# Kernel tuning notes

Measured on AMD Instinct MI355X. Metric: run time of the kernel, lower is better.

The kernel has to match this reference:

```python
import jax, jax.numpy as jnp
import numpy as np

B, S, D = 2, 2048, 1024
H = 16
HD = D // H  # head_dim = 64


def setup_inputs() -> dict:
    key = jax.random.key(0)
    ks = jax.random.split(key, 9)
    std = 1.0 / np.sqrt(HD)
    inp = {
        "X": jax.random.normal(ks[0], (B, S, D), dtype=jnp.float32),
        # per-head Q/K/V Linear weights stacked: [H, head_dim, head_dim], biases [H, head_dim]
        "Wq": jax.random.uniform(ks[1], (H, HD, HD), jnp.float32, -std, std),
        "bq": jax.random.uniform(ks[2], (H, HD), jnp.float32, -std, std),
        "Wk": jax.random.uniform(ks[3], (H, HD, HD), jnp.float32, -std, std),
        "bk": jax.random.uniform(ks[4], (H, HD), jnp.float32, -std, std),
        "Wv": jax.random.uniform(ks[5], (H, HD, HD), jnp.float32, -std, std),
        "bv": jax.random.uniform(ks[6], (H, HD), jnp.float32, -std, std),
        # output projection: [D, D] (in, out layout), bias [D]
        "Wo": jax.random.uniform(ks[7], (D, D), jnp.float32, -1.0 / np.sqrt(D), 1.0 / np.sqrt(D)),
        "bo": jax.random.uniform(ks[8], (D,), jnp.float32, -1.0 / np.sqrt(D), 1.0 / np.sqrt(D)),
    }
    return inp


def reference(X, Wq, bq, Wk, bk, Wv, bv, Wo, bo):
    # Split hidden dim into heads: [B, S, H, HD]
    x = X.reshape(B, S, H, HD)
    scale = jnp.sqrt(jnp.asarray(HD, dtype=X.dtype))
    # Per-head linear projections (batched over heads)
    Q = jnp.einsum("bshd,hde->bshe", x, Wq) + bq
    K = jnp.einsum("bshd,hde->bshe", x, Wk) + bk
    V = jnp.einsum("bshd,hde->bshe", x, Wv) + bv
    # Attention scores [B, H, S, S]
    scores = jnp.einsum("bshd,bthd->bhst", Q, K) / scale
    attn = jax.nn.softmax(scores, axis=-1)
    # Weighted values -> [B, S, H, HD] -> concat -> [B, S, D]
    out = jnp.einsum("bhst,bthd->bshd", attn, V).reshape(B, S, D)
    return out @ Wo + bo
```

## Files before the change

### kernel.cpp

```cpp
#include <hip/hip_runtime.h>
#include <stdint.h>

#define B_  2
#define S_  2048
#define D_  1024
#define H_  16
#define HD_ 64
#define TOK (B_*S_)

typedef __bf16 bf16x8 __attribute__((ext_vector_type(8)));
typedef __bf16 bf16x4 __attribute__((ext_vector_type(4)));
typedef float  f32x4  __attribute__((ext_vector_type(4)));

static_assert(sizeof(bf16x8) == 16, "bf16x8 must be 16B");
static_assert(sizeof(bf16x4) == 8,  "bf16x4 must be 8B");

__device__ __forceinline__ float fexp2(float x) { return __builtin_amdgcn_exp2f(x); }

__device__ __forceinline__ f32x4 mfma16(bf16x8 a, bf16x8 b, f32x4 c) {
    return __builtin_amdgcn_mfma_f32_16x16x32_bf16(a, b, c, 0, 0, 0);
}

__global__ __launch_bounds__(256) void k_transpose_wo(
    const float* __restrict__ Wo, unsigned short* __restrict__ WoT)
{
    __shared__ float t[64][65];
    const int i0 = blockIdx.x * 64;
    const int o0 = blockIdx.y * 64;
    const int tid = threadIdx.x;
    #pragma unroll
    for (int p = 0; p < 16; ++p) {
        int idx = tid + p * 256;
        int r = idx >> 6, c = idx & 63;
        t[r][c] = Wo[(size_t)(i0 + r) * D_ + o0 + c];
    }
    __syncthreads();
    #pragma unroll
    for (int p = 0; p < 16; ++p) {
        int idx = tid + p * 256;
        int r = idx >> 6, c = idx & 63;
        reinterpret_cast<__bf16*>(WoT)[(size_t)(o0 + r) * D_ + i0 + c] = (__bf16)t[c][r];
    }
}

__global__ __launch_bounds__(256) void k_qkv(
    const float* __restrict__ X,
    const float* __restrict__ Wq, const float* __restrict__ bq,
    const float* __restrict__ Wk, const float* __restrict__ bk,
    const float* __restrict__ Wv, const float* __restrict__ bv,
    unsigned short* __restrict__ Qo, unsigned short* __restrict__ Ko,
    unsigned short* __restrict__ Vt)
{
    __shared__ float          Wf[64][65];
    __shared__ unsigned short Xl[128 * 64];
    __shared__ unsigned short Wl[64 * 64];

    const int tid  = threadIdx.x;
    const int lane = tid & 63, w = tid >> 6;
    const int g = lane >> 4, q = lane & 15;
    const int tok0 = blockIdx.x * 128;
    const int h    = blockIdx.y;
    const int z    = blockIdx.z;
    const float* W  = (z == 0) ? Wq : (z == 1) ? Wk : Wv;
    const float* bb = (z == 0) ? bq : (z == 1) ? bk : bv;

    #pragma unroll
    for (int i = 0; i < 4; ++i) {
        int c = tid + 256 * i;
        int r = c >> 4, c4 = (c & 15) * 4;
        *reinterpret_cast<float4*>(&Wf[r][c4]) =
            *reinterpret_cast<const float4*>(&W[h * 4096 + r * 64 + c4]);
    }
    #pragma unroll
    for (int i = 0; i < 4; ++i) {
        int c = tid + 256 * i;
        int row = c >> 3, slot = c & 7;
        const float* src = &X[(size_t)(tok0 + row) * D_ + h * HD_ + slot * 8];
        float4 x0 = *reinterpret_cast<const float4*>(src);
        float4 x1 = *reinterpret_cast<const float4*>(src + 4);
        bf16x8 v = { (__bf16)x0.x, (__bf16)x0.y, (__bf16)x0.z, (__bf16)x0.w,
                     (__bf16)x1.x, (__bf16)x1.y, (__bf16)x1.z, (__bf16)x1.w };
        *reinterpret_cast<bf16x8*>(
            reinterpret_cast<char*>(Xl) + row * 128 + ((slot ^ (row & 7)) * 16)) = v;
    }
    __syncthreads();

    #pragma unroll
    for (int i = 0; i < 2; ++i) {
        int c = tid + 256 * i;
        int e = c >> 3, slot = c & 7;
        bf16x8 v;
        #pragma unroll
        for (int j = 0; j < 8; ++j) v[j] = (__bf16)Wf[slot * 8 + j][e];
        *reinterpret_cast<bf16x8*>(
            reinterpret_cast<char*>(Wl) + e * 128 + ((slot ^ (e & 7)) * 16)) = v;
    }
    __syncthreads();

    f32x4 acc[2][4] = {};
    #pragma unroll
    for (int s = 0; s < 2; ++s) {
        bf16x8 af[2], bfr[4];
        #pragma unroll
        for (int am = 0; am < 2; ++am) {
            int row  = w * 32 + am * 16 + q;
            int slot = (s * 4 + g) ^ (row & 7);
            af[am] = *reinterpret_cast<const bf16x8*>(
                reinterpret_cast<const char*>(Xl) + row * 128 + slot * 16);
        }
        #pragma unroll
        for (int bn = 0; bn < 4; ++bn) {
            int row  = bn * 16 + q;
            int slot = (s * 4 + g) ^ (row & 7);
            bfr[bn] = *reinterpret_cast<const bf16x8*>(
                reinterpret_cast<const char*>(Wl) + row * 128 + slot * 16);
        }
        #pragma unroll
        for (int am = 0; am < 2; ++am)
            #pragma unroll
            for (int bn = 0; bn < 4; ++bn)
                acc[am][bn] = mfma16(af[am], bfr[bn], acc[am][bn]);
    }

    const float scq = 0.18033688011112042f;
    const int b  = tok0 >> 11;
    const int sb = (tok0 & (S_ - 1)) + w * 32;
    #pragma unroll
    for (int bn = 0; bn < 4; ++bn) {
        int e = bn * 16 + q;
        float bia = bb[h * HD_ + e];
        #pragma unroll
        for (int am = 0; am < 2; ++am) {
            int s4 = sb + am * 16 + 4 * g;
            if (z == 2) {
                bf16x4 ov = { (__bf16)(acc[am][bn][0] + bia), (__bf16)(acc[am][bn][1] + bia),
                              (__bf16)(acc[am][bn][2] + bia), (__bf16)(acc[am][bn][3] + bia) };
                *reinterpret_cast<bf16x4*>(
                    &Vt[((size_t)(b * H_ + h) * HD_ + e) * S_ + s4]) = ov;
            } else {
                float sc = (z == 0) ? scq : 1.0f;
                unsigned short* dst = (z == 0) ? Qo : Ko;
                __bf16* d16 = reinterpret_cast<__bf16*>(dst);
                #pragma unroll
                for (int j = 0; j < 4; ++j)
                    d16[((size_t)(b * H_ + h) * S_ + s4 + j) * HD_ + e] =
                        (__bf16)((acc[am][bn][j] + bia) * sc);
            }
        }
    }
}

__global__ __launch_bounds__(256) void k_attn(
    const unsigned short* __restrict__ Q,
    const unsigned short* __restrict__ K,
    const unsigned short* __restrict__ V,
    unsigned short* __restrict__ O)
{
    __shared__ unsigned short K_lds[2][32 * 72];
    __shared__ unsigned short V_lds[2][64 * 40];
    __shared__ unsigned short P_lds[4][16 * 40];

    const int bh = blockIdx.y;
    const unsigned short* Qp = Q + (size_t)bh * S_ * HD_;
    const unsigned short* Kp = K + (size_t)bh * S_ * HD_;
    const unsigned short* Vp = V + (size_t)bh * HD_ * S_;

    const int tid  = threadIdx.x;
    const int lane = tid & 63, w = tid >> 6;
    const int g = lane >> 4, q = lane & 15;
    const int q0 = blockIdx.x * 64 + w * 16;

    bf16x8 qf0 = *reinterpret_cast<const bf16x8*>(&Qp[(size_t)(q0 + q) * HD_ + 8 * g]);
    bf16x8 qf1 = *reinterpret_cast<const bf16x8*>(&Qp[(size_t)(q0 + q) * HD_ + 32 + 8 * g]);

    f32x4 acc0 = {0.f, 0.f, 0.f, 0.f}, acc1 = acc0, acc2 = acc0, acc3 = acc0;
    float m = -3.0e38f, lp = 0.0f;

    const int kr = tid >> 3, ks = (tid & 7) * 8;
    const int vr = tid >> 2, vs = (tid & 3) * 8;
    unsigned short* Pw = P_lds[w];

    const unsigned short* kSrc = Kp + (size_t)kr * HD_ + ks;
    const unsigned short* vSrc = Vp + (size_t)vr * S_  + vs;

    {
        uint4 k0 = *reinterpret_cast<const uint4*>(kSrc);
        uint4 v0 = *reinterpret_cast<const uint4*>(vSrc);
        *reinterpret_cast<uint4*>(&K_lds[0][kr * 72 + ks]) = k0;
        *reinterpret_cast<uint4*>(&V_lds[0][vr * 40 + vs]) = v0;
    }
    __syncthreads();

    const int NT = S_ / 32;
    for (int t = 0; t < NT; ++t) {
        const int cur = t & 1, nxt = cur ^ 1;

        uint4 kn, vn;
        const bool more = (t + 1 < NT);
        if (more) {
            kn = *reinterpret_cast<const uint4*>(kSrc + (size_t)(t + 1) * 32 * HD_);
            vn = *reinterpret_cast<const uint4*>(vSrc + (size_t)(t + 1) * 32);
        }

        const unsigned short* Kb = K_lds[cur];
        const unsigned short* Vb = V_lds[cur];
        bf16x8 k00 = *reinterpret_cast<const bf16x8*>(&Kb[q * 72 + 8 * g]);
        bf16x8 k01 = *reinterpret_cast<const bf16x8*>(&Kb[q * 72 + 32 + 8 * g]);
        bf16x8 k10 = *reinterpret_cast<const bf16x8*>(&Kb[(16 + q) * 72 + 8 * g]);
        bf16x8 k11 = *reinterpret_cast<const bf16x8*>(&Kb[(16 + q) * 72 + 32 + 8 * g]);
        bf16x8 vf0 = *reinterpret_cast<const bf16x8*>(&Vb[(0 * 16 + q) * 40 + 8 * g]);
        bf16x8 vf1 = *reinterpret_cast<const bf16x8*>(&Vb[(1 * 16 + q) * 40 + 8 * g]);
        bf16x8 vf2 = *reinterpret_cast<const bf16x8*>(&Vb[(2 * 16 + q) * 40 + 8 * g]);
        bf16x8 vf3 = *reinterpret_cast<const bf16x8*>(&Vb[(3 * 16 + q) * 40 + 8 * g]);

        f32x4 z4 = {0.f, 0.f, 0.f, 0.f};
        f32x4 s0 = mfma16(k00, qf0, z4); s0 = mfma16(k01, qf1, s0);
        f32x4 s1 = mfma16(k10, qf0, z4); s1 = mfma16(k11, qf1, s1);

        float pmax = fmaxf(fmaxf(fmaxf(s0[0], s0[1]), fmaxf(s0[2], s0[3])),
                           fmaxf(fmaxf(s1[0], s1[1]), fmaxf(s1[2], s1[3])));
        if (!__all(pmax - m <= 8.0f)) {
            float pm = pmax;
            pm = fmaxf(pm, __shfl_xor(pm, 16));
            pm = fmaxf(pm, __shfl_xor(pm, 32));
            float mn  = fmaxf(m, pm);
            float scl = fexp2(m - mn);
            m = mn;
            lp *= scl;
            acc0 *= scl; acc1 *= scl; acc2 *= scl; acc3 *= scl;
        }
        float p0 = fexp2(s0[0] - m), p1 = fexp2(s0[1] - m);
        float p2 = fexp2(s0[2] - m), p3 = fexp2(s0[3] - m);
        float p4 = fexp2(s1[0] - m), p5 = fexp2(s1[1] - m);
        float p6 = fexp2(s1[2] - m), p7 = fexp2(s1[3] - m);
        lp += ((p0 + p1) + (p2 + p3)) + ((p4 + p5) + (p6 + p7));

        bf16x4 pa = { (__bf16)p0, (__bf16)p1, (__bf16)p2, (__bf16)p3 };
        bf16x4 pb = { (__bf16)p4, (__bf16)p5, (__bf16)p6, (__bf16)p7 };
        *reinterpret_cast<bf16x4*>(&Pw[q * 40 + 4 * g])      = pa;
        *reinterpret_cast<bf16x4*>(&Pw[q * 40 + 16 + 4 * g]) = pb;

        bf16x8 pf = *reinterpret_cast<const bf16x8*>(&Pw[q * 40 + 8 * g]);
        acc0 = mfma16(vf0, pf, acc0);
        acc1 = mfma16(vf1, pf, acc1);
        acc2 = mfma16(vf2, pf, acc2);
        acc3 = mfma16(vf3, pf, acc3);

        if (more) {
            *reinterpret_cast<uint4*>(&K_lds[nxt][kr * 72 + ks]) = kn;
            *reinterpret_cast<uint4*>(&V_lds[nxt][vr * 40 + vs]) = vn;
        }
        __syncthreads();
    }

    lp += __shfl_xor(lp, 16);
    lp += __shfl_xor(lp, 32);
    const float inv = 1.0f / lp;
    const int b = bh >> 4, h = bh & 15;
    size_t row = (size_t)(b * S_ + q0 + q) * D_ + h * HD_ + 4 * g;
    __bf16* Ob = reinterpret_cast<__bf16*>(O);
    bf16x4 o0 = { (__bf16)(acc0[0]*inv), (__bf16)(acc0[1]*inv),
                  (__bf16)(acc0[2]*inv), (__bf16)(acc0[3]*inv) };
    bf16x4 o1 = { (__bf16)(acc1[0]*inv), (__bf16)(acc1[1]*inv),
                  (__bf16)(acc1[2]*inv), (__bf16)(acc1[3]*inv) };
    bf16x4 o2 = { (__bf16)(acc2[0]*inv), (__bf16)(acc2[1]*inv),
                  (__bf16)(acc2[2]*inv), (__bf16)(acc2[3]*inv) };
    bf16x4 o3 = { (__bf16)(acc3[0]*inv), (__bf16)(acc3[1]*inv),
                  (__bf16)(acc3[2]*inv), (__bf16)(acc3[3]*inv) };
    *reinterpret_cast<bf16x4*>(&Ob[row + 0])  = o0;
    *reinterpret_cast<bf16x4*>(&Ob[row + 16]) = o1;
    *reinterpret_cast<bf16x4*>(&Ob[row + 32]) = o2;
    *reinterpret_cast<bf16x4*>(&Ob[row + 48]) = o3;
}

__global__ __launch_bounds__(256) void k_out(
    const unsigned short* __restrict__ A,
    const unsigned short* __restrict__ Wt,
    const float* __restrict__ bo,
    float* __restrict__ C)
{
    __shared__ unsigned short Al[2][128 * 64];
    __shared__ unsigned short Bl[2][128 * 64];

    const int tid  = threadIdx.x;
    const int lane = tid & 63, w = tid >> 6;
    const int g = lane >> 4, q = lane & 15;
    const int wr = w & 1, wc = w >> 1;
    const int m0 = blockIdx.x * 128;
    const int n0 = blockIdx.y * 128;

    int    sbyte[4];
    size_t sgA[4], sgB[4];
    #pragma unroll
    for (int i = 0; i < 4; ++i) {
        int c = tid + 256 * i;
        int row = c >> 3, slot = c & 7;
        sbyte[i] = row * 128 + ((slot ^ (row & 7)) * 16);
        sgA[i] = (size_t)(m0 + row) * D_ + slot * 8;
        sgB[i] = (size_t)(n0 + row) * D_ + slot * 8;
    }

    uint4 ra[4], rb[4];
    #pragma unroll
    for (int i = 0; i < 4; ++i) {
        ra[i] = *reinterpret_cast<const uint4*>(A  + sgA[i]);
        rb[i] = *reinterpret_cast<const uint4*>(Wt + sgB[i]);
    }
    #pragma unroll
    for (int i = 0; i < 4; ++i) {
        *reinterpret_cast<uint4*>(reinterpret_cast<char*>(Al[0]) + sbyte[i]) = ra[i];
        *reinterpret_cast<uint4*>(reinterpret_cast<char*>(Bl[0]) + sbyte[i]) = rb[i];
    }
    __syncthreads();

    f32x4 acc[4][4] = {};
    const int NKT = D_ / 64;
    for (int kt = 0; kt < NKT; ++kt) {
        const int cur = kt & 1, nxt = cur ^ 1;
        const bool more = (kt + 1 < NKT);
        if (more) {
            #pragma unroll
            for (int i = 0; i < 4; ++i) {
                ra[i] = *reinterpret_cast<const uint4*>(A  + sgA[i] + (kt + 1) * 64);
                rb[i] = *reinterpret_cast<const uint4*>(Wt + sgB[i] + (kt + 1) * 64);
            }
        }
        const char* Ab = reinterpret_cast<const char*>(Al[cur]);
        const char* Bb = reinterpret_cast<const char*>(Bl[cur]);
        #pragma unroll
        for (int s = 0; s < 2; ++s) {
            bf16x8 af[4], bfr[4];
            #pragma unroll
            for (int am = 0; am < 4; ++am) {
                int row  = wr * 64 + am * 16 + q;
                int slot = (s * 4 + g) ^ (row & 7);
                af[am] = *reinterpret_cast<const bf16x8*>(Ab + row * 128 + slot * 16);
            }
            #pragma unroll
            for (int bn = 0; bn < 4; ++bn) {
                int row  = wc * 64 + bn * 16 + q;
                int slot = (s * 4 + g) ^ (row & 7);
                bfr[bn] = *reinterpret_cast<const bf16x8*>(Bb + row * 128 + slot * 16);
            }
            #pragma unroll
            for (int am = 0; am < 4; ++am)
                #pragma unroll
                for (int bn = 0; bn < 4; ++bn)
                    acc[am][bn] = mfma16(af[am], bfr[bn], acc[am][bn]);
        }
        if (more) {
            #pragma unroll
            for (int i = 0; i < 4; ++i) {
                *reinterpret_cast<uint4*>(reinterpret_cast<char*>(Al[nxt]) + sbyte[i]) = ra[i];
                *reinterpret_cast<uint4*>(reinterpret_cast<char*>(Bl[nxt]) + sbyte[i]) = rb[i];
            }
        }
        __syncthreads();
    }

    #pragma unroll
    for (int bn = 0; bn < 4; ++bn) {
        int n = n0 + wc * 64 + bn * 16 + q;
        float bia = bo[n];
        #pragma unroll
        for (int am = 0; am < 4; ++am) {
            int mbase = m0 + wr * 64 + am * 16 + 4 * g;
            #pragma unroll
            for (int j = 0; j < 4; ++j)
                C[(size_t)(mbase + j) * D_ + n] = acc[am][bn][j] + bia;
        }
    }
}

extern "C" void kernel_launch(void* const* d_in, const int* in_sizes, int n_in,
                              void* d_out, int out_size, void* d_ws, size_t ws_size,
                              hipStream_t stream)
{
    const float* X  = (const float*)d_in[0];
    const float* Wq = (const float*)d_in[1];
    const float* bq = (const float*)d_in[2];
    const float* Wk = (const float*)d_in[3];
    const float* bk = (const float*)d_in[4];
    const float* Wv = (const float*)d_in[5];
    const float* bv = (const float*)d_in[6];
    const float* Wo = (const float*)d_in[7];
    const float* bo = (const float*)d_in[8];
    float* out = (float*)d_out;

    unsigned short* ws = (unsigned short*)d_ws;
    const size_t QN = (size_t)B_ * H_ * S_ * HD_;
    unsigned short* Qb  = ws;
    unsigned short* Kb  = ws + QN;
    unsigned short* Vtb = ws + 2 * QN;
    unsigned short* Ob  = ws + 3 * QN;
    unsigned short* WoT = ws + 4 * QN;

    k_transpose_wo<<<dim3(16, 16), 256, 0, stream>>>(Wo, WoT);
    k_qkv<<<dim3(TOK / 128, H_, 3), 256, 0, stream>>>(X, Wq, bq, Wk, bk, Wv, bv, Qb, Kb, Vtb);
    k_attn<<<dim3(S_ / 64, B_ * H_), 256, 0, stream>>>(Qb, Kb, Vtb, Ob);
    k_out<<<dim3(TOK / 128, D_ / 128), 256, 0, stream>>>(Ob, WoT, bo, out);
}
```

Measured before the change: 180.9 us.

## Fuse Q/K/V projections per block and process two query tiles per attention wave

The QKV projection now loads and converts each X tile once and computes Q, K and V in one block, using weights pre-transposed to bf16 by a new small kernel. This removes the repeated X reads and the per-block weight transpose. Q/K stores are vectorized by swapping MFMA operand order. The attention kernel gives each wave 32 query rows instead of 16, reusing each K/V LDS fragment across two query tiles. That halves the grid and raises register and LDS pressure per block.

Result: slower. 186.7 us (+3.2%).

```diff
diff --git a/kernel.cpp b/kernel.cpp
--- a/kernel.cpp
+++ b/kernel.cpp
@@ -43,34 +43,49 @@
     }
 }
 
+__global__ __launch_bounds__(256) void k_transpose_w(
+    const float* __restrict__ Wq, const float* __restrict__ Wk,
+    const float* __restrict__ Wv, unsigned short* __restrict__ WT)
+{
+    __shared__ float t[64][65];
+    const int h = blockIdx.x, z = blockIdx.y;
+    const float* W = (z == 0) ? Wq : (z == 1) ? Wk : Wv;
+    const int tid = threadIdx.x;
+    #pragma unroll
+    for (int p = 0; p < 4; ++p) {
+        int idx = tid + p * 256;
+        int r = idx >> 4, c4 = (idx & 15) * 4;
+        *reinterpret_cast<float4*>(&t[r][c4]) =
+            *reinterpret_cast<const float4*>(&W[h * 4096 + r * 64 + c4]);
+    }
+    __syncthreads();
+    const int e = tid >> 2, db = (tid & 3) * 16;
+    __bf16* out = reinterpret_cast<__bf16*>(WT) + ((size_t)(z * H_ + h) * 64 + e) * 64 + db;
+    #pragma unroll
+    for (int jj = 0; jj < 2; ++jj) {
+        bf16x8 v;
+        #pragma unroll
+        for (int j = 0; j < 8; ++j) v[j] = (__bf16)t[db + jj * 8 + j][e];
+        *reinterpret_cast<bf16x8*>(out + jj * 8) = v;
+    }
+}
+
 __global__ __launch_bounds__(256) void k_qkv(
-    const float* __restrict__ X,
-    const float* __restrict__ Wq, const float* __restrict__ bq,
-    const float* __restrict__ Wk, const float* __restrict__ bk,
-    const float* __restrict__ Wv, const float* __restrict__ bv,
+    const float* __restrict__ X, const unsigned short* __restrict__ WT,
+    const float* __restrict__ bq, const float* __restrict__ bk,
+    const float* __restrict__ bv,
     unsigned short* __restrict__ Qo, unsigned short* __restrict__ Ko,
     unsigned short* __restrict__ Vt)
 {
-    __shared__ float          Wf[64][65];
     __shared__ unsigned short Xl[128 * 64];
-    __shared__ unsigned short Wl[64 * 64];
+    __shared__ unsigned short Wl[3][64 * 64];
 
     const int tid  = threadIdx.x;
     const int lane = tid & 63, w = tid >> 6;
     const int g = lane >> 4, q = lane & 15;
     const int tok0 = blockIdx.x * 128;
     const int h    = blockIdx.y;
-    const int z    = blockIdx.z;
-    const float* W  = (z == 0) ? Wq : (z == 1) ? Wk : Wv;
-    const float* bb = (z == 0) ? bq : (z == 1) ? bk : bv;
-
-    #pragma unroll
-    for (int i = 0; i < 4; ++i) {
-        int c = tid + 256 * i;
-        int r = c >> 4, c4 = (c & 15) * 4;
-        *reinterpret_cast<float4*>(&Wf[r][c4]) =
-            *reinterpret_cast<const float4*>(&W[h * 4096 + r * 64 + c4]);
-    }
+
     #pragma unroll
     for (int i = 0; i < 4; ++i) {
         int c = tid + 256 * i;
@@ -83,68 +98,89 @@
         *reinterpret_cast<bf16x8*>(
             reinterpret_cast<char*>(Xl) + row * 128 + ((slot ^ (row & 7)) * 16)) = v;
     }
+    #pragma unroll
+    for (int zz = 0; zz < 3; ++zz) {
+        #pragma unroll
+        for (int i = 0; i < 2; ++i) {
+            int c = tid + 256 * i;
+            int e = c >> 3, slot = c & 7;
+            bf16x8 v = *reinterpret_cast<const bf16x8*>(
+                &WT[((size_t)(zz * H_ + h) * 64 + e) * 64 + slot * 8]);
+            *reinterpret_cast<bf16x8*>(
+                reinterpret_cast<char*>(Wl[zz]) + e * 128 + ((slot ^ (e & 7)) * 16)) = v;
+        }
+    }
     __syncthreads();
-
-    #pragma unroll
-    for (int i = 0; i < 2; ++i) {
-        int c = tid + 256 * i;
-        int e = c >> 3, slot = c & 7;
-        bf16x8 v;
-        #pragma unroll
-        for (int j = 0; j < 8; ++j) v[j] = (__bf16)Wf[slot * 8 + j][e];
-        *reinterpret_cast<bf16x8*>(
-            reinterpret_cast<char*>(Wl) + e * 128 + ((slot ^ (e & 7)) * 16)) = v;
-    }
-    __syncthreads();
-
-    f32x4 acc[2][4] = {};
-    #pragma unroll
-    for (int s = 0; s < 2; ++s) {
-        bf16x8 af[2], bfr[4];
-        #pragma unroll
-        for (int am = 0; am < 2; ++am) {
-            int row  = w * 32 + am * 16 + q;
-            int slot = (s * 4 + g) ^ (row & 7);
-            af[am] = *reinterpret_cast<const bf16x8*>(
-                reinterpret_cast<const char*>(Xl) + row * 128 + slot * 16);
-        }
-        #pragma unroll
-        for (int bn = 0; bn < 4; ++bn) {
-            int row  = bn * 16 + q;
-            int slot = (s * 4 + g) ^ (row & 7);
-            bfr[bn] = *reinterpret_cast<const bf16x8*>(
-                reinterpret_cast<const char*>(Wl) + row * 128 + slot * 16);
-        }
-        #pragma unroll
-        for (int am = 0; am < 2; ++am)
-            #pragma unroll
-            for (int bn = 0; bn < 4; ++bn)
-                acc[am][bn] = mfma16(af[am], bfr[bn], acc[am][bn]);
-    }
 
     const float scq = 0.18033688011112042f;
     const int b  = tok0 >> 11;
     const int sb = (tok0 & (S_ - 1)) + w * 32;
-    #pragma unroll
-    for (int bn = 0; bn < 4; ++bn) {
-        int e = bn * 16 + q;
-        float bia = bb[h * HD_ + e];
+
+    #pragma unroll
+    for (int z = 0; z < 3; ++z) {
+        const float* bb = (z == 0) ? bq : (z == 1) ? bk : bv;
+        f32x4 acc[2][4] = {};
         #pragma unroll
-        for (int am = 0; am < 2; ++am) {
-            int s4 = sb + am * 16 + 4 * g;
+        for (int s = 0; s < 2; ++s) {
+            bf16x8 af[2], bfr[4];
+            #pragma unroll
+            for (int am = 0; am < 2; ++am) {
+                int row  = w * 32 + am * 16 + q;
+                int slot = (s * 4 + g) ^ (row & 7);
+                af[am] = *reinterpret_cast<const bf16x8*>(
+                    reinterpret_cast<const char*>(Xl) + row * 128 + slot * 16);
+            }
+            #pragma unroll
+            for (int bn = 0; bn < 4; ++bn) {
+                int row  = bn * 16 + q;
+                int slot = (s * 4 + g) ^ (row & 7);
+                bfr[bn] = *reinterpret_cast<const bf16x8*>(
+                    reinterpret_cast<const char*>(Wl[z]) + row * 128 + slot * 16);
+            }
             if (z == 2) {
-                bf16x4 ov = { (__bf16)(acc[am][bn][0] + bia), (__bf16)(acc[am][bn][1] + bia),
-                              (__bf16)(acc[am][bn][2] + bia), (__bf16)(acc[am][bn][3] + bia) };
-                *reinterpret_cast<bf16x4*>(
-                    &Vt[((size_t)(b * H_ + h) * HD_ + e) * S_ + s4]) = ov;
+                #pragma unroll
+                for (int am = 0; am < 2; ++am)
+                    #pragma unroll
+                    for (int bn = 0; bn < 4; ++bn)
+                        acc[am][bn] = mfma16(af[am], bfr[bn], acc[am][bn]);
             } else {
-                float sc = (z == 0) ? scq : 1.0f;
-                unsigned short* dst = (z == 0) ? Qo : Ko;
-                __bf16* d16 = reinterpret_cast<__bf16*>(dst);
                 #pragma unroll
-                for (int j = 0; j < 4; ++j)
-                    d16[((size_t)(b * H_ + h) * S_ + s4 + j) * HD_ + e] =
-                        (__bf16)((acc[am][bn][j] + bia) * sc);
+                for (int am = 0; am < 2; ++am)
+                    #pragma unroll
+                    for (int bn = 0; bn < 4; ++bn)
+                        acc[am][bn] = mfma16(bfr[bn], af[am], acc[am][bn]);
+            }
+        }
+        if (z == 2) {
+            #pragma unroll
+            for (int bn = 0; bn < 4; ++bn) {
+                int e = bn * 16 + q;
+                float bia = bb[h * HD_ + e];
+                #pragma unroll
+                for (int am = 0; am < 2; ++am) {
+                    int s4 = sb + am * 16 + 4 * g;
+                    bf16x4 ov = { (__bf16)(acc[am][bn][0] + bia), (__bf16)(acc[am][bn][1] + bia),
+                                  (__bf16)(acc[am][bn][2] + bia), (__bf16)(acc[am][bn][3] + bia) };
+                    *reinterpret_cast<bf16x4*>(
+                        &Vt[((size_t)(b * H_ + h) * HD_ + e) * S_ + s4]) = ov;
+                }
+            }
+        } else {
+            const float sc = (z == 0) ? scq : 1.0f;
+            unsigned short* dst = (z == 0) ? Qo : Ko;
+            #pragma unroll
+            for (int bn = 0; bn < 4; ++bn) {
+                float4 bia4 = *reinterpret_cast<const float4*>(&bb[h * HD_ + bn * 16 + 4 * g]);
+                #pragma unroll
+                for (int am = 0; am < 2; ++am) {
+                    int tok = sb + am * 16 + q;
+                    bf16x4 ov = { (__bf16)((acc[am][bn][0] + bia4.x) * sc),
+                                  (__bf16)((acc[am][bn][1] + bia4.y) * sc),
+                                  (__bf16)((acc[am][bn][2] + bia4.z) * sc),
+                                  (__bf16)((acc[am][bn][3] + bia4.w) * sc) };
+                    *reinterpret_cast<bf16x4*>(
+                        &dst[((size_t)(b * H_ + h) * S_ + tok) * HD_ + bn * 16 + 4 * g]) = ov;
+                }
             }
         }
     }
@@ -158,7 +194,7 @@
 {
     __shared__ unsigned short K_lds[2][32 * 72];
     __shared__ unsigned short V_lds[2][64 * 40];
-    __shared__ unsigned short P_lds[4][16 * 40];
+    __shared__ unsigned short P_lds[4][32 * 40];
 
     const int bh = blockIdx.y;
     const unsigned short* Qp = Q + (size_t)bh * S_ * HD_;
@@ -168,13 +204,16 @@
     const int tid  = threadIdx.x;
     const int lane = tid & 63, w = tid >> 6;
     const int g = lane >> 4, q = lane & 15;
-    const int q0 = blockIdx.x * 64 + w * 16;
-
-    bf16x8 qf0 = *reinterpret_cast<const bf16x8*>(&Qp[(size_t)(q0 + q) * HD_ + 8 * g]);
-    bf16x8 qf1 = *reinterpret_cast<const bf16x8*>(&Qp[(size_t)(q0 + q) * HD_ + 32 + 8 * g]);
-
-    f32x4 acc0 = {0.f, 0.f, 0.f, 0.f}, acc1 = acc0, acc2 = acc0, acc3 = acc0;
-    float m = -3.0e38f, lp = 0.0f;
+    const int q0   = blockIdx.x * 128 + w * 32;
+    const int rowA = q0 + q, rowB = q0 + 16 + q;
+
+    bf16x8 qfA0 = *reinterpret_cast<const bf16x8*>(&Qp[(size_t)rowA * HD_ + 8 * g]);
+    bf16x8 qfA1 = *reinterpret_cast<const bf16x8*>(&Qp[(size_t)rowA * HD_ + 32 + 8 * g]);
+    bf16x8 qfB0 = *reinterpret_cast<const bf16x8*>(&Qp[(size_t)rowB * HD_ + 8 * g]);
+    bf16x8 qfB1 = *reinterpret_cast<const bf16x8*>(&Qp[(size_t)rowB * HD_ + 32 + 8 * g]);
+
+    f32x4 accA[4] = {}, accB[4] = {};
+    float mA = -3.0e38f, mB = -3.0e38f, lA = 0.0f, lB = 0.0f;
 
     const int kr = tid >> 3, ks = (tid & 7) * 8;
     const int vr = tid >> 2, vs = (tid & 3) * 8;
@@ -214,37 +253,61 @@
         bf16x8 vf3 = *reinterpret_cast<const bf16x8*>(&Vb[(3 * 16 + q) * 40 + 8 * g]);
 
         f32x4 z4 = {0.f, 0.f, 0.f, 0.f};
-        f32x4 s0 = mfma16(k00, qf0, z4); s0 = mfma16(k01, qf1, s0);
-        f32x4 s1 = mfma16(k10, qf0, z4); s1 = mfma16(k11, qf1, s1);
-
-        float pmax = fmaxf(fmaxf(fmaxf(s0[0], s0[1]), fmaxf(s0[2], s0[3])),
-                           fmaxf(fmaxf(s1[0], s1[1]), fmaxf(s1[2], s1[3])));
-        if (!__all(pmax - m <= 8.0f)) {
-            float pm = pmax;
-            pm = fmaxf(pm, __shfl_xor(pm, 16));
-            pm = fmaxf(pm, __shfl_xor(pm, 32));
-            float mn  = fmaxf(m, pm);
-            float scl = fexp2(m - mn);
-            m = mn;
-            lp *= scl;
-            acc0 *= scl; acc1 *= scl; acc2 *= scl; acc3 *= scl;
-        }
-        float p0 = fexp2(s0[0] - m), p1 = fexp2(s0[1] - m);
-        float p2 = fexp2(s0[2] - m), p3 = fexp2(s0[3] - m);
-        float p4 = fexp2(s1[0] - m), p5 = fexp2(s1[1] - m);
-        float p6 = fexp2(s1[2] - m), p7 = fexp2(s1[3] - m);
-        lp += ((p0 + p1) + (p2 + p3)) + ((p4 + p5) + (p6 + p7));
-
-        bf16x4 pa = { (__bf16)p0, (__bf16)p1, (__bf16)p2, (__bf16)p3 };
-        bf16x4 pb = { (__bf16)p4, (__bf16)p5, (__bf16)p6, (__bf16)p7 };
-        *reinterpret_cast<bf16x4*>(&Pw[q * 40 + 4 * g])      = pa;
-        *reinterpret_cast<bf16x4*>(&Pw[q * 40 + 16 + 4 * g]) = pb;
-
-        bf16x8 pf = *reinterpret_cast<const bf16x8*>(&Pw[q * 40 + 8 * g]);
-        acc0 = mfma16(vf0, pf, acc0);
-        acc1 = mfma16(vf1, pf, acc1);
-        acc2 = mfma16(vf2, pf, acc2);
-        acc3 = mfma16(vf3, pf, acc3);
+        f32x4 sA0 = mfma16(k00, qfA0, z4); sA0 = mfma16(k01, qfA1, sA0);
+        f32x4 sA1 = mfma16(k10, qfA0, z4); sA1 = mfma16(k11, qfA1, sA1);
+        f32x4 sB0 = mfma16(k00, qfB0, z4); sB0 = mfma16(k01, qfB1, sB0);
+        f32x4 sB1 = mfma16(k10, qfB0, z4); sB1 = mfma16(k11, qfB1, sB1);
+
+        float pmA = fmaxf(fmaxf(fmaxf(sA0[0], sA0[1]), fmaxf(sA0[2], sA0[3])),
+                          fmaxf(fmaxf(sA1[0], sA1[1]), fmaxf(sA1[2], sA1[3])));
+        float pmB = fmaxf(fmaxf(fmaxf(sB0[0], sB0[1]), fmaxf(sB0[2], sB0[3])),
+                          fmaxf(fmaxf(sB1[0], sB1[1]), fmaxf(sB1[2], sB1[3])));
+        if (!__all((pmA - mA <= 8.0f) && (pmB - mB <= 8.0f))) {
+            float rA = pmA;
+            rA = fmaxf(rA, __shfl_xor(rA, 16));
+            rA = fmaxf(rA, __shfl_xor(rA, 32));
+            float mnA = fmaxf(mA, rA);
+            float sclA = fexp2(mA - mnA);
+            mA = mnA; lA *= sclA;
+            accA[0] *= sclA; accA[1] *= sclA; accA[2] *= sclA; accA[3] *= sclA;
+            float rB = pmB;
+            rB = fmaxf(rB, __shfl_xor(rB, 16));
+            rB = fmaxf(rB, __shfl_xor(rB, 32));
+            float mnB = fmaxf(mB, rB);
+            float sclB = fexp2(mB - mnB);
+            mB = mnB; lB *= sclB;
+            accB[0] *= sclB; accB[1] *= sclB; accB[2] *= sclB; accB[3] *= sclB;
+        }
+        float pA0 = fexp2(sA0[0] - mA), pA1 = fexp2(sA0[1] - mA);
+        float pA2 = fexp2(sA0[2] - mA), pA3 = fexp2(sA0[3] - mA);
+        float pA4 = fexp2(sA1[0] - mA), pA5 = fexp2(sA1[1] - mA);
+        float pA6 = fexp2(sA1[2] - mA), pA7 = fexp2(sA1[3] - mA);
+        float pB0 = fexp2(sB0[0] - mB), pB1 = fexp2(sB0[1] - mB);
+        float pB2 = fexp2(sB0[2] - mB), pB3 = fexp2(sB0[3] - mB);
+        float pB4 = fexp2(sB1[0] - mB), pB5 = fexp2(sB1[1] - mB);
+        float pB6 = fexp2(sB1[2] - mB), pB7 = fexp2(sB1[3] - mB);
+        lA += ((pA0 + pA1) + (pA2 + pA3)) + ((pA4 + pA5) + (pA6 + pA7));
+        lB += ((pB0 + pB1) + (pB2 + pB3)) + ((pB4 + pB5) + (pB6 + pB7));
+
+        bf16x4 a0 = { (__bf16)pA0, (__bf16)pA1, (__bf16)pA2, (__bf16)pA3 };
+        bf16x4 a1 = { (__bf16)pA4, (__bf16)pA5, (__bf16)pA6, (__bf16)pA7 };
+        bf16x4 b0 = { (__bf16)pB0, (__bf16)pB1, (__bf16)pB2, (__bf16)pB3 };
+        bf16x4 b1 = { (__bf16)pB4, (__bf16)pB5, (__bf16)pB6, (__bf16)pB7 };
+        *reinterpret_cast<bf16x4*>(&Pw[q * 40 + 4 * g])             = a0;
+        *reinterpret_cast<bf16x4*>(&Pw[q * 40 + 16 + 4 * g])        = a1;
+        *reinterpret_cast<bf16x4*>(&Pw[(16 + q) * 40 + 4 * g])      = b0;
+        *reinterpret_cast<bf16x4*>(&Pw[(16 + q) * 40 + 16 + 4 * g]) = b1;
+
+        bf16x8 pfA = *reinterpret_cast<const bf16x8*>(&Pw[q * 40 + 8 * g]);
+        bf16x8 pfB = *reinterpret_cast<const bf16x8*>(&Pw[(16 + q) * 40 + 8 * g]);
+        accA[0] = mfma16(vf0, pfA, accA[0]);
+        accA[1] = mfma16(vf1, pfA, accA[1]);
+        accA[2] = mfma16(vf2, pfA, accA[2]);
+        accA[3] = mfma16(vf3, pfA, accA[3]);
+        accB[0] = mfma16(vf0, pfB, accB[0]);
+        accB[1] = mfma16(vf1, pfB, accB[1]);
+        accB[2] = mfma16(vf2, pfB, accB[2]);
+        accB[3] = mfma16(vf3, pfB, accB[3]);
 
         if (more) {
             *reinterpret_cast<uint4*>(&K_lds[nxt][kr * 72 + ks]) = kn;
@@ -253,24 +316,22 @@
         __syncthreads();
     }
 
-    lp += __shfl_xor(lp, 16);
-    lp += __shfl_xor(lp, 32);
-    const float inv = 1.0f / lp;
+    lA += __shfl_xor(lA, 16);  lA += __shfl_xor(lA, 32);
+    lB += __shfl_xor(lB, 16);  lB += __shfl_xor(lB, 32);
+    const float invA = 1.0f / lA, invB = 1.0f / lB;
     const int b = bh >> 4, h = bh & 15;
-    size_t row = (size_t)(b * S_ + q0 + q) * D_ + h * HD_ + 4 * g;
     __bf16* Ob = reinterpret_cast<__bf16*>(O);
-    bf16x4 o0 = { (__bf16)(acc0[0]*inv), (__bf16)(acc0[1]*inv),
-                  (__bf16)(acc0[2]*inv), (__bf16)(acc0[3]*inv) };
-    bf16x4 o1 = { (__bf16)(acc1[0]*inv), (__bf16)(acc1[1]*inv),
-                  (__bf16)(acc1[2]*inv), (__bf16)(acc1[3]*inv) };
-    bf16x4 o2 = { (__bf16)(acc2[0]*inv), (__bf16)(acc2[1]*inv),
-                  (__bf16)(acc2[2]*inv), (__bf16)(acc2[3]*inv) };
-    bf16x4 o3 = { (__bf16)(acc3[0]*inv), (__bf16)(acc3[1]*inv),
-                  (__bf16)(acc3[2]*inv), (__bf16)(acc3[3]*inv) };
-    *reinterpret_cast<bf16x4*>(&Ob[row + 0])  = o0;
-    *reinterpret_cast<bf16x4*>(&Ob[row + 16]) = o1;
-    *reinterpret_cast<bf16x4*>(&Ob[row + 32]) = o2;
-    *reinterpret_cast<bf16x4*>(&Ob[row + 48]) = o3;
+    size_t rA_ = (size_t)(b * S_ + rowA) * D_ + h * HD_ + 4 * g;
+    size_t rB_ = (size_t)(b * S_ + rowB) * D_ + h * HD_ + 4 * g;
+    #pragma unroll
+    for (int d = 0; d < 4; ++d) {
+        bf16x4 oa = { (__bf16)(accA[d][0]*invA), (__bf16)(accA[d][1]*invA),
+                      (__bf16)(accA[d][2]*invA), (__bf16)(accA[d][3]*invA) };
+        bf16x4 ob = { (__bf16)(accB[d][0]*invB), (__bf16)(accB[d][1]*invB),
+                      (__bf16)(accB[d][2]*invB), (__bf16)(accB[d][3]*invB) };
+        *reinterpret_cast<bf16x4*>(&Ob[rA_ + 16 * d]) = oa;
+        *reinterpret_cast<bf16x4*>(&Ob[rB_ + 16 * d]) = ob;
+    }
 }
 
 __global__ __launch_bounds__(256) void k_out(
@@ -389,14 +450,16 @@
 
     unsigned short* ws = (unsigned short*)d_ws;
     const size_t QN = (size_t)B_ * H_ * S_ * HD_;
-    unsigned short* Qb  = ws;
-    unsigned short* Kb  = ws + QN;
-    unsigned short* Vtb = ws + 2 * QN;
-    unsigned short* Ob  = ws + 3 * QN;
-    unsigned short* WoT = ws + 4 * QN;
+    unsigned short* Qb    = ws;
+    unsigned short* Kb    = ws + QN;
+    unsigned short* Vtb   = ws + 2 * QN;
+    unsigned short* Ob    = ws + 3 * QN;
+    unsigned short* WoT   = ws + 4 * QN;
+    unsigned short* WqkvT = ws + 4 * QN + (size_t)D_ * D_;
 
     k_transpose_wo<<<dim3(16, 16), 256, 0, stream>>>(Wo, WoT);
-    k_qkv<<<dim3(TOK / 128, H_, 3), 256, 0, stream>>>(X, Wq, bq, Wk, bk, Wv, bv, Qb, Kb, Vtb);
-    k_attn<<<dim3(S_ / 64, B_ * H_), 256, 0, stream>>>(Qb, Kb, Vtb, Ob);
+    k_transpose_w<<<dim3(H_, 3), 256, 0, stream>>>(Wq, Wk, Wv, WqkvT);
+    k_qkv<<<dim3(TOK / 128, H_), 256, 0, stream>>>(X, WqkvT, bq, bk, bv, Qb, Kb, Vtb);
+    k_attn<<<dim3(S_ / 128, B_ * H_), 256, 0, stream>>>(Qb, Kb, Vtb, Ob);
     k_out<<<dim3(TOK / 128, D_ / 128), 256, 0, stream>>>(Ob, WoT, bo, out);
 }
```
